# Performance work log

Hardware: AMD Instinct MI355X
Metric: run time of the kernel (lower is better)

## Reference

```python
import math
import jax, jax.numpy as jnp
import numpy as np

BLOCK = 256
LAYER_IDX = 5
NUM_HIDDEN_LAYERS = 32


def get_slopes(head_dim):
    equ = lambda x: 1 / 2 ** (8 / x)
    log2 = math.log2(head_dim)
    if log2.is_integer():
        return [equ(head_dim) ** i for i in range(1, head_dim + 1)]
    lower = 2 ** math.floor(log2)
    upper = 2 ** math.ceil(log2)
    ls = get_slopes(lower)
    us = get_slopes(upper)
    return ls + us[::2][: head_dim - lower]


def setup_inputs() -> dict:
    key = jax.random.key(0)
    k1, k2, k3 = jax.random.split(key, 3)
    B, H, S, D = 2, 64, 4096, 64
    q = jax.random.normal(k1, (B, H, S, D), dtype=jnp.float32)
    k = jax.random.normal(k2, (B, H, S, D), dtype=jnp.float32)
    v = jax.random.normal(k3, (B, H, S, D), dtype=jnp.float32)
    mask = jnp.ones((B, S), dtype=jnp.int32)
    return {"query_states": q, "key_states": k, "value_states": v, "attention_mask": mask}


def _lightning_attention(q, k, v, attention_mask):
    B, H, S, D = q.shape
    E = v.shape[-1]
    # mask padded positions in values
    v = v * attention_mask[:, None, :, None].astype(v.dtype)

    # per-head decay slopes, scaled by layer depth (note: H == D by construction)
    slopes = np.asarray(get_slopes(D), dtype=np.float32)
    slopes = slopes * (1.0 - LAYER_IDX / (NUM_HIDDEN_LAYERS - 1) + 1e-05)
    slope = jnp.asarray(slopes)[:, None, None]  # [H, 1, 1]

    arr = jnp.arange(1, BLOCK + 1, dtype=jnp.float32)
    q_decay = jnp.exp(-slope * arr[:, None])            # [H, BLOCK, 1]
    k_decay = jnp.exp(-slope * (BLOCK - arr)[:, None])  # [H, BLOCK, 1]
    idx = arr[:, None] - arr[None, :]                   # [BLOCK, BLOCK]
    s_idx = slope * idx[None]                           # [H, BLOCK, BLOCK] (slope [H,1,1] broadcasts)
    diag_decay = jnp.exp(jnp.where(idx[None] >= 0, -s_idx, -jnp.inf))  # [H, BLOCK, BLOCK]
    block_decay = jnp.exp(-slope * BLOCK)               # [H, 1, 1]

    nb = S // BLOCK
    qb = q.reshape(B, H, nb, BLOCK, D).transpose(2, 0, 1, 3, 4)  # [nb, B, H, BLOCK, D]
    kb = k.reshape(B, H, nb, BLOCK, D).transpose(2, 0, 1, 3, 4)
    vb = v.reshape(B, H, nb, BLOCK, E).transpose(2, 0, 1, 3, 4)

    def step(kv, blk):
        qi, ki, vi = blk  # each [B, H, BLOCK, D/E]
        # inter-block: decayed query reads recurrent kv state
        o_inter = jnp.einsum('bhmd,bhde->bhme', qi * q_decay, kv)
        # intra-block: causal decayed attention within the block
        qk = jnp.einsum('bhmd,bhnd->bhmn', qi, ki) * diag_decay
        o_intra = jnp.einsum('bhmn,bhne->bhme', qk, vi)
        # update recurrent state
        kv_new = block_decay * kv + jnp.einsum('bhmd,bhme->bhde', ki * k_decay, vi)
        return kv_new, o_inter + o_intra

    kv0 = jnp.zeros((B, H, D, E), dtype=jnp.float32)
    _, outs = jax.lax.scan(step, kv0, (qb, kb, vb))  # outs: [nb, B, H, BLOCK, E]
    out = outs.transpose(1, 2, 0, 3, 4).reshape(B, H, S, E)
    return out


def reference(query_states, key_states, value_states, attention_mask):
    return _lightning_attention(query_states, key_states, value_states, attention_mask)
```

## Files before the change

kernel.cpp:

```cpp
#include <hip/hip_runtime.h>

typedef __attribute__((ext_vector_type(4))) float f4;
typedef __attribute__((ext_vector_type(4))) float f32x4;
typedef __attribute__((ext_vector_type(8))) short short8;
typedef __attribute__((ext_vector_type(4))) short short4v;

#define S_  4096
#define NB_ 16
#define SLOPE_SCALE 0.838719677419355f

__device__ __forceinline__ float slope_for_head(int h) {
    return exp2f(-(float)(h + 1) * 0.125f) * SLOPE_SCALE;
}

__device__ __forceinline__ short f2bf(float f) {
    unsigned u = __float_as_uint(f);
    u += 0x7FFFu + ((u >> 16) & 1u);
    return (short)(u >> 16);
}
__device__ __forceinline__ float bf2f(short s) {
    return __uint_as_float(((unsigned)(unsigned short)s) << 16);
}

__device__ __forceinline__ int NX(int row, int n8) {
    return n8 ^ (((row >> 3) & 3) << 3);
}

template<int USE_KBF>
__global__ __launch_bounds__(256, 4) void phase1_kvblocks(
    const float* __restrict__ k, const float* __restrict__ v,
    const int* __restrict__ mask, float* __restrict__ kvt,
    short* __restrict__ vt, short* __restrict__ kbf)
{
    __shared__ float ks[32][64];
    __shared__ float vs[32][64];
    __shared__ short khi[64][40];
    __shared__ short klo[64][40];
    __shared__ short vhi[64][40];
    __shared__ short vlo[64][40];
    const int j  = blockIdx.x;
    const int bh = blockIdx.y;
    const int b  = bh >> 6;
    const int h  = bh & 63;
    const int t  = threadIdx.x;
    const int wave = t >> 6, lane = t & 63, quad = lane >> 4, l16 = lane & 15;
    const float slope = slope_for_head(h);

    const f32x4 zf = {0.f, 0.f, 0.f, 0.f};
    f32x4 acc[4];
    acc[0] = zf; acc[1] = zf; acc[2] = zf; acc[3] = zf;

    const long long tilebase = ((long long)bh * S_ + j * 256) * 64;
    const long long vtbase   = ((long long)(bh * NB_ + j)) * 16384;

    const int r0  = t >> 4;
    const int col = (t & 15) << 2;

    f4 kr0, kr1, vr0, vr1; int mr0, mr1;
    auto LOADSTG = [&](int ss) {
        long long g0 = tilebase + (long long)(ss * 32 + r0) * 64 + col;
        kr0 = *(const f4*)(k + g0);
        vr0 = *(const f4*)(v + g0);
        kr1 = *(const f4*)(k + g0 + 16 * 64);
        vr1 = *(const f4*)(v + g0 + 16 * 64);
        mr0 = mask[b * S_ + j * 256 + ss * 32 + r0];
        mr1 = mask[b * S_ + j * 256 + ss * 32 + r0 + 16];
    };
    LOADSTG(0);

    for (int ss = 0; ss < 8; ++ss) {
        {
            int gn0 = ss * 32 + r0;
            if (USE_KBF) {
                long long g0 = tilebase + (long long)gn0 * 64 + col;
                short4v kb0 = { f2bf(kr0.x), f2bf(kr0.y), f2bf(kr0.z), f2bf(kr0.w) };
                short4v kb1 = { f2bf(kr1.x), f2bf(kr1.y), f2bf(kr1.z), f2bf(kr1.w) };
                *(short4v*)(kbf + g0)           = kb0;
                *(short4v*)(kbf + g0 + 16 * 64) = kb1;
            }
            float kd0 = __expf(-slope * (float)(255 - gn0));
            float kd1 = __expf(-slope * (float)(255 - gn0 - 16));
            *(f4*)&ks[r0][col]      = kr0 * kd0;
            *(f4*)&ks[r0 + 16][col] = kr1 * kd1;
            *(f4*)&vs[r0][col]      = vr0 * (float)mr0;
            *(f4*)&vs[r0 + 16][col] = vr1 * (float)mr1;
        }
        if (ss < 7) LOADSTG(ss + 1);
        __syncthreads();

        {
            const int dl = lane;
            short8 k8h, k8l, v8h, v8l;
            #pragma unroll
            for (int rr = 0; rr < 8; ++rr) {
                float kx = ks[wave * 8 + rr][dl];
                short kh = f2bf(kx);
                k8h[rr] = kh; k8l[rr] = f2bf(kx - bf2f(kh));
                float vx = vs[wave * 8 + rr][dl];
                short vh = f2bf(vx);
                v8h[rr] = vh; v8l[rr] = f2bf(vx - bf2f(vh));
            }
            int ni = NX(dl, wave * 8);
            *(short8*)&khi[dl][ni] = k8h;
            *(short8*)&klo[dl][ni] = k8l;
            *(short8*)&vhi[dl][ni] = v8h;
            *(short8*)&vlo[dl][ni] = v8l;
        }
        __syncthreads();

        {
            int e  = t >> 2;
            int nb = (t & 3) << 3;
            short8 w = *(const short8*)&vhi[e][NX(e, nb)];
            *(short8*)(vt + vtbase + ss * 2048 + e * 32 + nb) = w;
        }

        {
            int ar = wave * 16 + l16;
            short8 ahi = *(const short8*)&vhi[ar][NX(ar, quad * 8)];
            short8 alo = *(const short8*)&vlo[ar][NX(ar, quad * 8)];
            #pragma unroll
            for (int dt = 0; dt < 4; ++dt) {
                int br = dt * 16 + l16;
                short8 bhi = *(const short8*)&khi[br][NX(br, quad * 8)];
                short8 blo = *(const short8*)&klo[br][NX(br, quad * 8)];
                acc[dt] = __builtin_amdgcn_mfma_f32_16x16x32_bf16(ahi, bhi, acc[dt], 0, 0, 0);
                acc[dt] = __builtin_amdgcn_mfma_f32_16x16x32_bf16(ahi, blo, acc[dt], 0, 0, 0);
                acc[dt] = __builtin_amdgcn_mfma_f32_16x16x32_bf16(alo, bhi, acc[dt], 0, 0, 0);
            }
        }
        __syncthreads();
    }

    float* o = kvt + ((long long)(bh * NB_ + j)) * 4096;
    #pragma unroll
    for (int dt = 0; dt < 4; ++dt) {
        #pragma unroll
        for (int r = 0; r < 4; ++r) {
            int e = wave * 16 + quad * 4 + r;
            o[e * 64 + dt * 16 + l16] = acc[dt][r];
        }
    }
}

template<int EMIT>
__global__ __launch_bounds__(256) void phase2_scan(float* __restrict__ kvt,
                                                   short* __restrict__ kvb)
{
    const int g    = blockIdx.x;
    const int bh   = g >> 2;
    const int part = g & 3;
    const int h    = bh & 63;
    const float slope = slope_for_head(h);
    const float bd = __expf(-slope * 256.0f);

    f4* base = (f4*)(kvt + (long long)bh * NB_ * 4096) + part * 256 + threadIdx.x;
    short* kb = kvb + (long long)bh * NB_ * 4096
              + ((long long)(part * 256 + threadIdx.x) << 2);
    f4 vals[NB_];
    #pragma unroll
    for (int jj = 0; jj < NB_; ++jj) vals[jj] = base[jj * 1024];
    f4 st = {0.f, 0.f, 0.f, 0.f};
    #pragma unroll
    for (int jj = 0; jj < NB_; ++jj) {
        base[jj * 1024] = st;
        if (EMIT) {
            short4v sb = { f2bf(st.x), f2bf(st.y), f2bf(st.z), f2bf(st.w) };
            *(short4v*)(kb + (long long)jj * 4096) = sb;
        }
        st = st * bd + vals[jj];
    }
}

template<int USE_KBF, int USE_KVB>
__global__ __launch_bounds__(256, 3) void phase3_output(
    const float* __restrict__ q, const float* __restrict__ kfp,
    const short* __restrict__ kbf, const float* __restrict__ kvt,
    const short* __restrict__ kvb, const short* __restrict__ vt,
    float* __restrict__ out)
{
    __shared__ short P[4][64 * 56];
    const int j    = blockIdx.x;
    const int bh   = blockIdx.y;
    const int h    = bh & 63;
    const int tid  = threadIdx.x;
    const int wave = tid >> 6;
    const int lane = tid & 63;
    const int quad = lane >> 4;
    const int l16  = lane & 15;
    const int wrole  = (wave + j) & 3;
    const float slope = slope_for_head(h);
    const int mwbase = wrole << 6;

    const long long rowbase = (long long)bh * S_ + j * 256 + mwbase;
    const long long kTile = ((long long)bh * S_ + j * 256) * 64;
    const long long vTile = ((long long)(bh * NB_ + j)) * 16384;

    short8 qf[4][2];
    #pragma unroll
    for (int mt = 0; mt < 4; ++mt) {
        const float* qp = q + (rowbase + mt * 16 + l16) * 64 + quad * 8;
        #pragma unroll
        for (int ks = 0; ks < 2; ++ks) {
            f4 a = *(const f4*)(qp + ks * 32);
            f4 b = *(const f4*)(qp + ks * 32 + 4);
            short8 f;
            f[0] = f2bf(a.x); f[1] = f2bf(a.y); f[2] = f2bf(a.z); f[3] = f2bf(a.w);
            f[4] = f2bf(b.x); f[5] = f2bf(b.y); f[6] = f2bf(b.z); f[7] = f2bf(b.w);
            qf[mt][ks] = f;
        }
    }

    auto LOADKF = [&](short8 (&dst)[2][2], int nb0) {
        #pragma unroll
        for (int nt = 0; nt < 2; ++nt) {
            const short* kp = kbf + kTile
                + (long long)(nb0 + nt * 16 + l16) * 64 + quad * 8;
            dst[nt][0] = *(const short8*)(kp);
            dst[nt][1] = *(const short8*)(kp + 32);
        }
    };

    short8 kfA[2][2];
    if (USE_KBF) LOADKF(kfA, 0);

    const f32x4 zf = {0.f, 0.f, 0.f, 0.f};
    f32x4 of[4][4];
    #pragma unroll
    for (int et = 0; et < 4; ++et)
        #pragma unroll
        for (int mt = 0; mt < 4; ++mt) of[et][mt] = zf;

    if (USE_KVB) {
        const short* kvbp = kvb + ((long long)(bh * NB_ + j) << 12);
        #pragma unroll
        for (int et = 0; et < 4; ++et) {
            #pragma unroll
            for (int ks = 0; ks < 2; ++ks) {
                short8 af = *(const short8*)(kvbp + (et * 16 + l16) * 64
                                             + ks * 32 + quad * 8);
                #pragma unroll
                for (int mt = 0; mt < 4; ++mt)
                    of[et][mt] = __builtin_amdgcn_mfma_f32_16x16x32_bf16(
                        af, qf[mt][ks], of[et][mt], 0, 0, 0);
            }
        }
    } else {
        const float* kvp = kvt + ((long long)(bh * NB_ + j) << 12);
        #pragma unroll
        for (int et = 0; et < 4; ++et) {
            #pragma unroll
            for (int ks = 0; ks < 2; ++ks) {
                const float* p = kvp + (et * 16 + l16) * 64 + ks * 32 + quad * 8;
                f4 a = *(const f4*)(p);
                f4 b = *(const f4*)(p + 4);
                short8 af;
                af[0] = f2bf(a.x); af[1] = f2bf(a.y); af[2] = f2bf(a.z); af[3] = f2bf(a.w);
                af[4] = f2bf(b.x); af[5] = f2bf(b.y); af[6] = f2bf(b.z); af[7] = f2bf(b.w);
                #pragma unroll
                for (int mt = 0; mt < 4; ++mt)
                    of[et][mt] = __builtin_amdgcn_mfma_f32_16x16x32_bf16(
                        af, qf[mt][ks], of[et][mt], 0, 0, 0);
            }
        }
    }
    #pragma unroll
    for (int mt = 0; mt < 4; ++mt) {
        float qd = __expf(-slope * (float)(mwbase + mt * 16 + l16 + 1));
        #pragma unroll
        for (int et = 0; et < 4; ++et) of[et][mt] *= qd;
    }

    const float er1 = __expf(slope);
    const float er2 = er1 * er1;
    const float er3 = er2 * er1;
    const float L  = __expf(-slope * (float)(l16 - quad * 4));
    const float T1 = __expf(-slope * 16.f);
    const float Ti = __expf(slope * 16.f);
    const float Tm[4] = {1.f, T1, T1 * T1, T1 * T1 * T1};

    short* Pw = &P[wave][0];
    const int nchunks = (mwbase >> 5) + 2;

    for (int c = 0; c < nchunks; ++c) {
        const int nbase = c << 5;
        const bool havenext = (c + 1 < nchunks);

        short8 va[4];
        #pragma unroll
        for (int et = 0; et < 4; ++et)
            va[et] = *(const short8*)(vt + vTile + c * 2048
                                      + (et * 16 + l16) * 32 + quad * 8);

        short8 kfB[2][2];
        if (USE_KBF && havenext) LOADKF(kfB, nbase + 32);

        if (!USE_KBF) {
            #pragma unroll
            for (int nt = 0; nt < 2; ++nt) {
                const float* kp = kfp + kTile
                    + (long long)(nbase + nt * 16 + l16) * 64 + quad * 8;
                #pragma unroll
                for (int ks = 0; ks < 2; ++ks) {
                    f4 a = *(const f4*)(kp + ks * 32);
                    f4 b = *(const f4*)(kp + ks * 32 + 4);
                    short8 f;
                    f[0] = f2bf(a.x); f[1] = f2bf(a.y); f[2] = f2bf(a.z); f[3] = f2bf(a.w);
                    f[4] = f2bf(b.x); f[5] = f2bf(b.y); f[6] = f2bf(b.z); f[7] = f2bf(b.w);
                    kfA[nt][ks] = f;
                }
            }
        }

        f32x4 sf[2][4];
        #pragma unroll
        for (int nt = 0; nt < 2; ++nt)
            #pragma unroll
            for (int mt = 0; mt < 4; ++mt) sf[nt][mt] = zf;
        #pragma unroll
        for (int nt = 0; nt < 2; ++nt)
            #pragma unroll
            for (int ks = 0; ks < 2; ++ks)
                #pragma unroll
                for (int mt = 0; mt < 4; ++mt)
                    sf[nt][mt] = __builtin_amdgcn_mfma_f32_16x16x32_bf16(
                        kfA[nt][ks], qf[mt][ks], sf[nt][mt], 0, 0, 0);

        const float WL = __expf(-slope * (float)(mwbase - nbase)) * L;
        #pragma unroll
        for (int nt = 0; nt < 2; ++nt) {
            #pragma unroll
            for (int mt = 0; mt < 4; ++mt) {
                int n0 = nbase + nt * 16 + quad * 4;
                int m  = mwbase + mt * 16 + l16;
                float ddb = WL * Tm[mt];
                if (nt) ddb *= Ti;
                f32x4 s = sf[nt][mt];
                float v0 = (m >= n0)     ? s[0] * ddb       : 0.f;
                float v1 = (m >= n0 + 1) ? s[1] * ddb * er1 : 0.f;
                float v2 = (m >= n0 + 2) ? s[2] * ddb * er2 : 0.f;
                float v3 = (m >= n0 + 3) ? s[3] * ddb * er3 : 0.f;
                short4v pk = {f2bf(v0), f2bf(v1), f2bf(v2), f2bf(v3)};
                *(short4v*)&Pw[(mt * 16 + l16) * 56 + nt * 16 + quad * 4] = pk;
            }
        }
        asm volatile("s_waitcnt lgkmcnt(0)" ::: "memory");

        short8 pb[4];
        #pragma unroll
        for (int mt = 0; mt < 4; ++mt)
            pb[mt] = *(const short8*)&Pw[(mt * 16 + l16) * 56 + quad * 8];

        #pragma unroll
        for (int et = 0; et < 4; ++et)
            #pragma unroll
            for (int mt = 0; mt < 4; ++mt)
                of[et][mt] = __builtin_amdgcn_mfma_f32_16x16x32_bf16(
                    va[et], pb[mt], of[et][mt], 0, 0, 0);

        if (USE_KBF && havenext) {
            #pragma unroll
            for (int nt = 0; nt < 2; ++nt) {
                kfA[nt][0] = kfB[nt][0];
                kfA[nt][1] = kfB[nt][1];
            }
        }
    }

    #pragma unroll
    for (int mt = 0; mt < 4; ++mt) {
        float* orow = out + (rowbase + mt * 16 + l16) * 64;
        #pragma unroll
        for (int et = 0; et < 4; ++et) {
            f4 o = {of[et][mt][0], of[et][mt][1], of[et][mt][2], of[et][mt][3]};
            *(f4*)(orow + et * 16 + quad * 4) = o;
        }
    }
}

extern "C" void kernel_launch(void* const* d_in, const int* in_sizes, int n_in,
                              void* d_out, int out_size, void* d_ws, size_t ws_size,
                              hipStream_t stream) {
    const float* q    = (const float*)d_in[0];
    const float* k    = (const float*)d_in[1];
    const float* v    = (const float*)d_in[2];
    const int*   mask = (const int*)d_in[3];
    float* kvt = (float*)d_ws;
    short* vt  = (short*)((char*)d_ws + (size_t)33554432);
    short* kbf = (short*)((char*)d_ws + (size_t)100663296);
    short* kvb = (short*)((char*)d_ws + (size_t)167772160);
    float* out = (float*)d_out;

    if (ws_size >= (size_t)184549376) {
        phase1_kvblocks<1><<<dim3(16, 128), 256, 0, stream>>>(k, v, mask, kvt, vt, kbf);
        phase2_scan<1><<<512, 256, 0, stream>>>(kvt, kvb);
        phase3_output<1, 1><<<dim3(16, 128), 256, 0, stream>>>(q, k, kbf, kvt, kvb, vt, out);
    } else if (ws_size >= (size_t)167772160) {
        phase1_kvblocks<1><<<dim3(16, 128), 256, 0, stream>>>(k, v, mask, kvt, vt, kbf);
        phase2_scan<0><<<512, 256, 0, stream>>>(kvt, kvb);
        phase3_output<1, 0><<<dim3(16, 128), 256, 0, stream>>>(q, k, kbf, kvt, kvb, vt, out);
    } else {
        phase1_kvblocks<0><<<dim3(16, 128), 256, 0, stream>>>(k, v, mask, kvt, vt, kbf);
        phase2_scan<0><<<512, 256, 0, stream>>>(kvt, kvb);
        phase3_output<0, 0><<<dim3(16, 128), 256, 0, stream>>>(q, k, kbf, kvt, kvb, vt, out);
    }
}
```

Baseline: 496.2 us.

## Load K/V column-wise into registers, skipping fp32 LDS staging in phase1

Phase 1 now has each lane load eight rows of one column straight into registers. It applies the key decay from a precomputed power table and the mask there, splits the values into bf16 hi/lo and writes them directly to the transposed LDS tiles and to the vt buffer. This removes the fp32 LDS staging arrays, one barrier and the LDS readback per sub-tile. The costs are scalar, less vectorized global loads, a second global read of K for the bf16 copy, and barriers that only wait on LDS traffic. The decay is now computed as a product of exponentials, which may differ slightly in rounding.

```diff
diff --git a/kernel.cpp b/kernel.cpp
--- a/kernel.cpp
+++ b/kernel.cpp
@@ -25,6 +25,12 @@
 __device__ __forceinline__ int NX(int row, int n8) {
     return n8 ^ (((row >> 3) & 3) << 3);
 }
+
+#define LDS_BAR() do {                                        \
+    asm volatile("s_waitcnt lgkmcnt(0)" ::: "memory");        \
+    __builtin_amdgcn_s_barrier();                             \
+    __builtin_amdgcn_sched_barrier(0);                        \
+} while (0)
 
 template<int USE_KBF>
 __global__ __launch_bounds__(256, 4) void phase1_kvblocks(
@@ -32,8 +38,6 @@
     const int* __restrict__ mask, float* __restrict__ kvt,
     short* __restrict__ vt, short* __restrict__ kbf)
 {
-    __shared__ float ks[32][64];
-    __shared__ float vs[32][64];
     __shared__ short khi[64][40];
     __shared__ short klo[64][40];
     __shared__ short vhi[64][40];
@@ -46,74 +50,70 @@
     const int wave = t >> 6, lane = t & 63, quad = lane >> 4, l16 = lane & 15;
     const float slope = slope_for_head(h);
 
+    const float er = __expf(slope);
+    float erp[8];
+    erp[0] = 1.f;
+    #pragma unroll
+    for (int jj = 1; jj < 8; ++jj) erp[jj] = erp[jj - 1] * er;
+
     const f32x4 zf = {0.f, 0.f, 0.f, 0.f};
     f32x4 acc[4];
     acc[0] = zf; acc[1] = zf; acc[2] = zf; acc[3] = zf;
 
     const long long tilebase = ((long long)bh * S_ + j * 256) * 64;
     const long long vtbase   = ((long long)(bh * NB_ + j)) * 16384;
-
-    const int r0  = t >> 4;
-    const int col = (t & 15) << 2;
-
-    f4 kr0, kr1, vr0, vr1; int mr0, mr1;
-    auto LOADSTG = [&](int ss) {
-        long long g0 = tilebase + (long long)(ss * 32 + r0) * 64 + col;
-        kr0 = *(const f4*)(k + g0);
-        vr0 = *(const f4*)(v + g0);
-        kr1 = *(const f4*)(k + g0 + 16 * 64);
-        vr1 = *(const f4*)(v + g0 + 16 * 64);
-        mr0 = mask[b * S_ + j * 256 + ss * 32 + r0];
-        mr1 = mask[b * S_ + j * 256 + ss * 32 + r0 + 16];
+    const int mbase = b * S_ + j * 256;
+
+    const int r0   = t >> 4;
+    const int colr = (t & 15) << 2;
+
+    float kc[8], vc[8], kn[8], vn[8];
+    float mk[8], mn[8];
+
+    auto LOADC = [&](int ss, float* kcd, float* vcd, float* mm) {
+        const long long g = tilebase + (long long)(ss * 32 + wave * 8) * 64 + lane;
+        #pragma unroll
+        for (int jj = 0; jj < 8; ++jj) {
+            kcd[jj] = k[g + jj * 64];
+            vcd[jj] = v[g + jj * 64];
+            mm[jj]  = (float)mask[mbase + ss * 32 + wave * 8 + jj];
+        }
     };
-    LOADSTG(0);
+    LOADC(0, kc, vc, mk);
 
     for (int ss = 0; ss < 8; ++ss) {
-        {
-            int gn0 = ss * 32 + r0;
-            if (USE_KBF) {
-                long long g0 = tilebase + (long long)gn0 * 64 + col;
-                short4v kb0 = { f2bf(kr0.x), f2bf(kr0.y), f2bf(kr0.z), f2bf(kr0.w) };
-                short4v kb1 = { f2bf(kr1.x), f2bf(kr1.y), f2bf(kr1.z), f2bf(kr1.w) };
-                *(short4v*)(kbf + g0)           = kb0;
-                *(short4v*)(kbf + g0 + 16 * 64) = kb1;
-            }
-            float kd0 = __expf(-slope * (float)(255 - gn0));
-            float kd1 = __expf(-slope * (float)(255 - gn0 - 16));
-            *(f4*)&ks[r0][col]      = kr0 * kd0;
-            *(f4*)&ks[r0 + 16][col] = kr1 * kd1;
-            *(f4*)&vs[r0][col]      = vr0 * (float)mr0;
-            *(f4*)&vs[r0 + 16][col] = vr1 * (float)mr1;
-        }
-        if (ss < 7) LOADSTG(ss + 1);
-        __syncthreads();
-
-        {
-            const int dl = lane;
-            short8 k8h, k8l, v8h, v8l;
-            #pragma unroll
-            for (int rr = 0; rr < 8; ++rr) {
-                float kx = ks[wave * 8 + rr][dl];
-                short kh = f2bf(kx);
-                k8h[rr] = kh; k8l[rr] = f2bf(kx - bf2f(kh));
-                float vx = vs[wave * 8 + rr][dl];
-                short vh = f2bf(vx);
-                v8h[rr] = vh; v8l[rr] = f2bf(vx - bf2f(vh));
-            }
-            int ni = NX(dl, wave * 8);
-            *(short8*)&khi[dl][ni] = k8h;
-            *(short8*)&klo[dl][ni] = k8l;
-            *(short8*)&vhi[dl][ni] = v8h;
-            *(short8*)&vlo[dl][ni] = v8l;
-        }
-        __syncthreads();
-
-        {
-            int e  = t >> 2;
-            int nb = (t & 3) << 3;
-            short8 w = *(const short8*)&vhi[e][NX(e, nb)];
-            *(short8*)(vt + vtbase + ss * 2048 + e * 32 + nb) = w;
-        }
+        const float kdb = __expf(-slope * (float)(255 - ss * 32 - wave * 8));
+        short8 k8h, k8l, v8h, v8l;
+        #pragma unroll
+        for (int jj = 0; jj < 8; ++jj) {
+            float kx = kc[jj] * (kdb * erp[jj]);
+            short kh = f2bf(kx);
+            k8h[jj] = kh; k8l[jj] = f2bf(kx - bf2f(kh));
+            float vx = vc[jj] * mk[jj];
+            short vh = f2bf(vx);
+            v8h[jj] = vh; v8l[jj] = f2bf(vx - bf2f(vh));
+        }
+        const int ni = NX(lane, wave * 8);
+        *(short8*)&khi[lane][ni] = k8h;
+        *(short8*)&klo[lane][ni] = k8l;
+        *(short8*)&vhi[lane][ni] = v8h;
+        *(short8*)&vlo[lane][ni] = v8l;
+
+        *(short8*)(vt + vtbase + ss * 2048 + lane * 32 + wave * 8) = v8h;
+
+        if (USE_KBF) {
+            long long g0 = tilebase + (long long)(ss * 32 + r0) * 64 + colr;
+            f4 kk0 = *(const f4*)(k + g0);
+            f4 kk1 = *(const f4*)(k + g0 + 1024);
+            short4v b0 = { f2bf(kk0.x), f2bf(kk0.y), f2bf(kk0.z), f2bf(kk0.w) };
+            short4v b1 = { f2bf(kk1.x), f2bf(kk1.y), f2bf(kk1.z), f2bf(kk1.w) };
+            *(short4v*)(kbf + g0)        = b0;
+            *(short4v*)(kbf + g0 + 1024) = b1;
+        }
+
+        if (ss < 7) LOADC(ss + 1, kn, vn, mn);
+
+        LDS_BAR();
 
         {
             int ar = wave * 16 + l16;
@@ -129,7 +129,15 @@
                 acc[dt] = __builtin_amdgcn_mfma_f32_16x16x32_bf16(alo, bhi, acc[dt], 0, 0, 0);
             }
         }
-        __syncthreads();
+
+        LDS_BAR();
+
+        if (ss < 7) {
+            #pragma unroll
+            for (int jj = 0; jj < 8; ++jj) {
+                kc[jj] = kn[jj]; vc[jj] = vn[jj]; mk[jj] = mn[jj];
+            }
+        }
     }
 
     float* o = kvt + ((long long)(bh * NB_ + j)) * 4096;
```

Measured after the change: 498.0 us. About the same (+0.4%).
